# Kernel optimization log

Hardware: AMD Instinct MI355X
Metric: run time of the kernel (lower is better)

The kernel has to match this reference:

```python
import jax, jax.numpy as jnp
import numpy as np

B, F0, D = 4096, 39, 16
CROSS_LAYER_SIZE = (128, 128)


def _he_uniform(key, shape):
    fan_in = int(np.prod(shape[:-1]))
    limit = np.sqrt(6.0 / fan_in)
    return jax.random.uniform(key, shape, jnp.float32, -limit, limit)


def setup_inputs() -> dict:
    key = jax.random.key(0)
    k_x, k_f0, k_f1, k_w, k_b = jax.random.split(key, 5)
    x = jax.random.normal(k_x, (B, F0, D), dtype=jnp.float32)
    # field_nums with direct=False: [39, 128//2=64, 64]
    f0 = _he_uniform(k_f0, (F0 * F0, CROSS_LAYER_SIZE[0]))          # (1521, 128)
    f1 = _he_uniform(k_f1, (F0 * (CROSS_LAYER_SIZE[0] // 2), CROSS_LAYER_SIZE[1]))  # (2496, 128)
    out_dim = CROSS_LAYER_SIZE[0] // 2 + CROSS_LAYER_SIZE[1]        # 192
    dense_w = _he_uniform(k_w, (out_dim, 1))
    dense_b = jnp.zeros((1,), dtype=jnp.float32)
    return {"x": x, "f0": f0, "f1": f1, "dense_w": dense_w, "dense_b": dense_b}


def reference(x, f0, f1, dense_w, dense_b):
    # CIN forward (direct=False, use_bias=False, use_residual=False, relu)
    # x: (B, F0, D)
    filters = [f0, f1]
    n_layers = len(CROSS_LAYER_SIZE)
    h = x  # hidden state, (B, Fk, D)
    finals = []
    for idx, L in enumerate(CROSS_LAYER_SIZE):
        Fk = h.shape[1]
        # filter f_ has shape (F0*Fk, L) with i (field of x0) major, j (field of h) minor
        Wr = filters[idx].reshape(F0, Fk, L)
        # fused outer product + conv1d (kernel width 1 == matmul over i,j):
        # z[b, m, d] = sum_{i,j} x[b,i,d] * h[b,j,d] * W[i,j,m]
        z = jnp.einsum('bid,bjd,ijm->bmd', x, h, Wr)  # (B, L, D)
        z = jax.nn.relu(z)
        if idx != n_layers - 1:
            # split along feature-map axis: first half feeds next layer,
            # second half goes to output
            h = z[:, : L // 2, :]
            finals.append(z[:, L // 2:, :])
        else:
            finals.append(z)
    result = jnp.sum(jnp.concatenate(finals, axis=1), axis=-1)  # (B, 192)
    return result @ dense_w + dense_b  # (B, 1)
```

## Files before the change

### kernel.cpp

```cpp
#include <hip/hip_runtime.h>


typedef __attribute__((ext_vector_type(8)))  short bf16x8;
typedef __attribute__((ext_vector_type(16))) float f32x16;

static __device__ __forceinline__ unsigned short f2bf_rne(float f) {
    unsigned int u = __builtin_bit_cast(unsigned int, f);
    u = (u + 0x7FFFu + ((u >> 16) & 1u)) >> 16;
    return (unsigned short)u;
}
static __device__ __forceinline__ unsigned int pk_trunc(float a, float b) {
    unsigned int ua = __builtin_bit_cast(unsigned int, a);
    unsigned int ub = __builtin_bit_cast(unsigned int, b);
    return (ua >> 16) | (ub & 0xffff0000u);
}

__global__ __launch_bounds__(256)
void CIN_repack(const float* __restrict__ f0, const float* __restrict__ f1,
                uint4* __restrict__ ws)
{
    const int tid  = blockIdx.x * 256 + threadIdx.x;
    const int n    = tid & 127;
    const int slot = tid >> 7;
    const int half = slot & 1;
    const int kh   = (slot >> 1) & 1;
    const int ch   = slot >> 2;
    float v[8];
    if (ch < 50) {
        const int ig = ch / 5, jg = ch - ig * 5;
        const int i = ig * 4 + kh * 2 + half;
        const bool iok = (i < 39);
#pragma unroll
        for (int t = 0; t < 8; ++t) {
            const int j = jg * 8 + t;
            v[t] = (iok && j < 39) ? f0[(i * 39 + j) * 128 + n] : 0.f;
        }
    } else {
        const int c1 = ch - 50;
        const int jg = c1 / 5, ig = c1 - jg * 5;
        const int j = jg * 4 + kh * 2 + half;
#pragma unroll
        for (int t = 0; t < 8; ++t) {
            const int i = ig * 8 + t;
            v[t] = (i < 39) ? f1[(i * 64 + j) * 128 + n] : 0.f;
        }
    }
    uint4 pk;
    pk.x = (unsigned int)f2bf_rne(v[0]) | ((unsigned int)f2bf_rne(v[1]) << 16);
    pk.y = (unsigned int)f2bf_rne(v[2]) | ((unsigned int)f2bf_rne(v[3]) << 16);
    pk.z = (unsigned int)f2bf_rne(v[4]) | ((unsigned int)f2bf_rne(v[5]) << 16);
    pk.w = (unsigned int)f2bf_rne(v[6]) | ((unsigned int)f2bf_rne(v[7]) << 16);
    const int lane = half * 32 + (n & 31);
    const int cg   = n >> 5;
    ws[ch * 512 + kh * 256 + cg * 64 + lane] = pk;
}

static __device__ __forceinline__ bf16x8 build8(float xi, float4 a, float4 b) {
    union { unsigned int u[4]; bf16x8 v; } r;
    r.u[0] = pk_trunc(xi * a.x, xi * a.y);
    r.u[1] = pk_trunc(xi * a.z, xi * a.w);
    r.u[2] = pk_trunc(xi * b.x, xi * b.y);
    r.u[3] = pk_trunc(xi * b.z, xi * b.w);
    return r.v;
}

__global__ __launch_bounds__(256, 2)
void CIN_main(const float* __restrict__ x,
              const char* __restrict__ wsB,
              const float* __restrict__ dw,
              const float* __restrict__ db,
              float* __restrict__ out)
{
    __shared__ __align__(16) float xsTd[8][16][44];
    __shared__ __align__(16) float hsT[8][64][17];
    __shared__ float dws[192];
    __shared__ float red[2][2][4];

    const int tid  = threadIdx.x;
    const int w    = tid >> 6;
    const int lane = tid & 63;
    const int g    = w & 1;
    const int hh   = w >> 1;
    const int half = lane >> 5;
    const int d    = lane & 15;
    const int bsel = (lane >> 4) & 1;
    const int g4   = g * 4;

    const char* wbase = wsB + lane * 16 + hh * 2048 + 2560;
    bf16x8 Bb[2][2][2];
    auto loadBg = [&](int ch, bf16x8 (&B)[2][2]) {
        const char* p0 = wbase + (size_t)ch * 8192;
        B[0][0] = *(const bf16x8*)(p0 - 2560);
        B[0][1] = *(const bf16x8*)(p0 - 1536);
        B[1][0] = *(const bf16x8*)(p0 + 1536);
        B[1][1] = *(const bf16x8*)(p0 + 2560);
    };

    loadBg(0, Bb[0]);
    loadBg(1, Bb[1]);

    const float4* xg4 = (const float4*)(x + (size_t)blockIdx.x * 8 * 624);
    for (int e4 = tid; e4 < 1248; e4 += 256) {
        float4 v = xg4[e4];
        int bb = e4 / 156, r = e4 - bb * 156;
        int i = r >> 2, d0 = (r & 3) * 4;
        xsTd[bb][d0 + 0][i] = v.x; xsTd[bb][d0 + 1][i] = v.y;
        xsTd[bb][d0 + 2][i] = v.z; xsTd[bb][d0 + 3][i] = v.w;
    }
    if (tid < 128) { int bb = tid >> 4, dd = tid & 15; xsTd[bb][dd][39] = 0.f; }
    if (tid < 192) dws[tid] = dw[tid];
    __syncthreads();

    float4 xv[2][10];
#pragma unroll
    for (int p = 0; p < 2; ++p) {
        const float* src = &xsTd[g4 + p * 2 + bsel][d][0];
#pragma unroll
        for (int q = 0; q < 10; ++q) xv[p][q] = *(const float4*)(src + q * 4);
    }

    f32x16 acc[2][2];
#pragma unroll
    for (int p = 0; p < 2; ++p)
#pragma unroll
        for (int c = 0; c < 2; ++c)
#pragma unroll
            for (int r = 0; r < 16; ++r) acc[p][c][r] = 0.f;

    float xiv[2][2];

#pragma unroll 1
    for (int o = 0; o < 5; ++o) {
#pragma unroll
        for (int u = 0; u < 10; ++u) {
            const int ch = o * 10 + u;
            const int jg = u % 5;
            if (jg == 0) {
                const int ib = (o * 2 + u / 5) * 4;
#pragma unroll
                for (int p = 0; p < 2; ++p)
#pragma unroll
                    for (int kh = 0; kh < 2; ++kh)
                        xiv[p][kh] = xsTd[g4 + p * 2 + bsel][d][ib + kh * 2 + half];
            }
            bf16x8 A[2][2];
#pragma unroll
            for (int p = 0; p < 2; ++p)
#pragma unroll
                for (int kh = 0; kh < 2; ++kh)
                    A[p][kh] = build8(xiv[p][kh], xv[p][jg * 2], xv[p][jg * 2 + 1]);
#pragma unroll
            for (int p = 0; p < 2; ++p)
#pragma unroll
                for (int c = 0; c < 2; ++c) {
                    acc[p][c] = __builtin_amdgcn_mfma_f32_32x32x16_bf16(A[p][0], Bb[u & 1][0][c], acc[p][c], 0, 0, 0);
                    acc[p][c] = __builtin_amdgcn_mfma_f32_32x32x16_bf16(A[p][1], Bb[u & 1][1][c], acc[p][c], 0, 0, 0);
                }
            loadBg(ch + 2, Bb[u & 1]);
        }
    }

    float cs[4] = {0.f, 0.f, 0.f, 0.f};
    if (hh == 0) {
#pragma unroll
        for (int p = 0; p < 2; ++p)
#pragma unroll
            for (int c = 0; c < 2; ++c)
#pragma unroll
                for (int r = 0; r < 16; ++r) {
                    const int row = (r & 3) + 8 * (r >> 2) + 4 * half;
                    hsT[g4 + p * 2 + (row >> 4)][c * 32 + (lane & 31)][row & 15] =
                        fmaxf(acc[p][c][r], 0.f);
                }
    } else {
#pragma unroll
        for (int p = 0; p < 2; ++p)
#pragma unroll
            for (int c = 0; c < 2; ++c) {
                const float dwv = dws[c * 32 + (lane & 31)];
#pragma unroll
                for (int r = 0; r < 16; ++r) {
                    const int row = (r & 3) + 8 * (r >> 2) + 4 * half;
                    cs[p * 2 + (row >> 4)] += fmaxf(acc[p][c][r], 0.f) * dwv;
                }
            }
    }
#pragma unroll
    for (int p = 0; p < 2; ++p)
#pragma unroll
        for (int c = 0; c < 2; ++c)
#pragma unroll
            for (int r = 0; r < 16; ++r) acc[p][c][r] = 0.f;
    __syncthreads();

#pragma unroll 1
    for (int o2 = 0; o2 < 8; ++o2) {
#pragma unroll
        for (int u = 0; u < 10; ++u) {
            const int ch = 50 + o2 * 10 + u;
            const int ig2 = u % 5;
            if (ig2 == 0) {
                const int jb = (o2 * 2 + u / 5) * 4;
#pragma unroll
                for (int p = 0; p < 2; ++p)
#pragma unroll
                    for (int kh = 0; kh < 2; ++kh)
                        xiv[p][kh] = hsT[g4 + p * 2 + bsel][jb + kh * 2 + half][d];
            }
            bf16x8 A[2][2];
#pragma unroll
            for (int p = 0; p < 2; ++p)
#pragma unroll
                for (int kh = 0; kh < 2; ++kh)
                    A[p][kh] = build8(xiv[p][kh], xv[p][ig2 * 2], xv[p][ig2 * 2 + 1]);
#pragma unroll
            for (int p = 0; p < 2; ++p)
#pragma unroll
                for (int c = 0; c < 2; ++c) {
                    acc[p][c] = __builtin_amdgcn_mfma_f32_32x32x16_bf16(A[p][0], Bb[u & 1][0][c], acc[p][c], 0, 0, 0);
                    acc[p][c] = __builtin_amdgcn_mfma_f32_32x32x16_bf16(A[p][1], Bb[u & 1][1][c], acc[p][c], 0, 0, 0);
                }
            int chn = ch + 2; if (chn > 129) chn = 129;
            loadBg(chn, Bb[u & 1]);
        }
    }

#pragma unroll
    for (int p = 0; p < 2; ++p)
#pragma unroll
        for (int c = 0; c < 2; ++c) {
            const float dwv = dws[64 + (2 * hh + c) * 32 + (lane & 31)];
#pragma unroll
            for (int r = 0; r < 16; ++r) {
                const int row = (r & 3) + 8 * (r >> 2) + 4 * half;
                cs[p * 2 + (row >> 4)] += fmaxf(acc[p][c][r], 0.f) * dwv;
            }
        }
#pragma unroll
    for (int rr = 0; rr < 4; ++rr)
#pragma unroll
        for (int off = 32; off > 0; off >>= 1)
            cs[rr] += __shfl_xor(cs[rr], off, 64);
    if (lane == 0) {
#pragma unroll
        for (int rr = 0; rr < 4; ++rr) red[g][hh][rr] = cs[rr];
    }
    __syncthreads();
    if (tid < 8) {
        const int g2 = tid >> 2, rr = tid & 3;
        out[blockIdx.x * 8 + g2 * 4 + rr] = red[g2][0][rr] + red[g2][1][rr] + db[0];
    }
}

extern "C" void kernel_launch(void* const* d_in, const int* in_sizes, int n_in,
                              void* d_out, int out_size, void* d_ws, size_t ws_size,
                              hipStream_t stream)
{
    const float* x  = (const float*)d_in[0];
    const float* f0 = (const float*)d_in[1];
    const float* f1 = (const float*)d_in[2];
    const float* dw = (const float*)d_in[3];
    const float* db = (const float*)d_in[4];
    float* out = (float*)d_out;

    CIN_repack<<<dim3(260), dim3(256), 0, stream>>>(f0, f1, (uint4*)d_ws);
    CIN_main<<<dim3(512), dim3(256), 0, stream>>>(x, (const char*)d_ws, dw, db, out);
}
```

Baseline: 130.6 us.

## Switch operands from bf16 to fp16 and build A with packed half multiplies

Weights are repacked as fp16 instead of bf16, and the MFMA calls move to the f16 32x32x16 variant. x and the hidden state are staged in LDS as fp16. The A fragments are built with packed half2 multiplies instead of scalar fp32 multiplies plus truncation. This cuts VALU work per MFMA and halves LDS footprint and traffic, but products are now rounded in fp16, which risks overflow or precision loss if values are large.

```diff
diff --git a/kernel.cpp b/kernel.cpp
--- a/kernel.cpp
+++ b/kernel.cpp
@@ -1,19 +1,9 @@
 #include <hip/hip_runtime.h>
 
 
-typedef __attribute__((ext_vector_type(8)))  short bf16x8;
+typedef _Float16 h2    __attribute__((ext_vector_type(2)));
+typedef _Float16 f16x8 __attribute__((ext_vector_type(8)));
 typedef __attribute__((ext_vector_type(16))) float f32x16;
-
-static __device__ __forceinline__ unsigned short f2bf_rne(float f) {
-    unsigned int u = __builtin_bit_cast(unsigned int, f);
-    u = (u + 0x7FFFu + ((u >> 16) & 1u)) >> 16;
-    return (unsigned short)u;
-}
-static __device__ __forceinline__ unsigned int pk_trunc(float a, float b) {
-    unsigned int ua = __builtin_bit_cast(unsigned int, a);
-    unsigned int ub = __builtin_bit_cast(unsigned int, b);
-    return (ua >> 16) | (ub & 0xffff0000u);
-}
 
 __global__ __launch_bounds__(256)
 void CIN_repack(const float* __restrict__ f0, const float* __restrict__ f1,
@@ -45,23 +35,13 @@
             v[t] = (i < 39) ? f1[(i * 64 + j) * 128 + n] : 0.f;
         }
     }
-    uint4 pk;
-    pk.x = (unsigned int)f2bf_rne(v[0]) | ((unsigned int)f2bf_rne(v[1]) << 16);
-    pk.y = (unsigned int)f2bf_rne(v[2]) | ((unsigned int)f2bf_rne(v[3]) << 16);
-    pk.z = (unsigned int)f2bf_rne(v[4]) | ((unsigned int)f2bf_rne(v[5]) << 16);
-    pk.w = (unsigned int)f2bf_rne(v[6]) | ((unsigned int)f2bf_rne(v[7]) << 16);
+    union { h2 h[4]; uint4 q; } pk;
+#pragma unroll
+    for (int t = 0; t < 4; ++t)
+        pk.h[t] = h2{(_Float16)v[2 * t], (_Float16)v[2 * t + 1]};
     const int lane = half * 32 + (n & 31);
     const int cg   = n >> 5;
-    ws[ch * 512 + kh * 256 + cg * 64 + lane] = pk;
-}
-
-static __device__ __forceinline__ bf16x8 build8(float xi, float4 a, float4 b) {
-    union { unsigned int u[4]; bf16x8 v; } r;
-    r.u[0] = pk_trunc(xi * a.x, xi * a.y);
-    r.u[1] = pk_trunc(xi * a.z, xi * a.w);
-    r.u[2] = pk_trunc(xi * b.x, xi * b.y);
-    r.u[3] = pk_trunc(xi * b.z, xi * b.w);
-    return r.v;
+    ws[ch * 512 + kh * 256 + cg * 64 + lane] = pk.q;
 }
 
 __global__ __launch_bounds__(256, 2)
@@ -71,8 +51,8 @@
               const float* __restrict__ db,
               float* __restrict__ out)
 {
-    __shared__ __align__(16) float xsTd[8][16][44];
-    __shared__ __align__(16) float hsT[8][64][17];
+    __shared__ __align__(16) _Float16 xsH[8][16][64];
+    __shared__ __align__(4)  _Float16 hsH[8][64][18];
     __shared__ float dws[192];
     __shared__ float red[2][2][4];
 
@@ -87,13 +67,13 @@
     const int g4   = g * 4;
 
     const char* wbase = wsB + lane * 16 + hh * 2048 + 2560;
-    bf16x8 Bb[2][2][2];
-    auto loadBg = [&](int ch, bf16x8 (&B)[2][2]) {
+    f16x8 Bb[2][2][2];
+    auto loadBg = [&](int ch, f16x8 (&B)[2][2]) {
         const char* p0 = wbase + (size_t)ch * 8192;
-        B[0][0] = *(const bf16x8*)(p0 - 2560);
-        B[0][1] = *(const bf16x8*)(p0 - 1536);
-        B[1][0] = *(const bf16x8*)(p0 + 1536);
-        B[1][1] = *(const bf16x8*)(p0 + 2560);
+        B[0][0] = *(const f16x8*)(p0 - 2560);
+        B[0][1] = *(const f16x8*)(p0 - 1536);
+        B[1][0] = *(const f16x8*)(p0 + 1536);
+        B[1][1] = *(const f16x8*)(p0 + 2560);
     };
 
     loadBg(0, Bb[0]);
@@ -104,19 +84,24 @@
         float4 v = xg4[e4];
         int bb = e4 / 156, r = e4 - bb * 156;
         int i = r >> 2, d0 = (r & 3) * 4;
-        xsTd[bb][d0 + 0][i] = v.x; xsTd[bb][d0 + 1][i] = v.y;
-        xsTd[bb][d0 + 2][i] = v.z; xsTd[bb][d0 + 3][i] = v.w;
-    }
-    if (tid < 128) { int bb = tid >> 4, dd = tid & 15; xsTd[bb][dd][39] = 0.f; }
+        xsH[bb][d0 + 0][i] = (_Float16)v.x; xsH[bb][d0 + 1][i] = (_Float16)v.y;
+        xsH[bb][d0 + 2][i] = (_Float16)v.z; xsH[bb][d0 + 3][i] = (_Float16)v.w;
+    }
+    if (tid < 128) { int bb = tid >> 4, dd = tid & 15; xsH[bb][dd][39] = (_Float16)0.f; }
     if (tid < 192) dws[tid] = dw[tid];
     __syncthreads();
 
-    float4 xv[2][10];
+    h2 xv[2][20];
 #pragma unroll
     for (int p = 0; p < 2; ++p) {
-        const float* src = &xsTd[g4 + p * 2 + bsel][d][0];
-#pragma unroll
-        for (int q = 0; q < 10; ++q) xv[p][q] = *(const float4*)(src + q * 4);
+        const uint4* src = (const uint4*)&xsH[g4 + p * 2 + bsel][d][0];
+#pragma unroll
+        for (int q5 = 0; q5 < 5; ++q5) {
+            union { uint4 q; h2 h[4]; } u;
+            u.q = src[q5];
+#pragma unroll
+            for (int t = 0; t < 4; ++t) xv[p][q5 * 4 + t] = u.h[t];
+        }
     }
 
     f32x16 acc[2][2];
@@ -127,7 +112,7 @@
 #pragma unroll
             for (int r = 0; r < 16; ++r) acc[p][c][r] = 0.f;
 
-    float xiv[2][2];
+    h2 xiv2[2][2];
 
 #pragma unroll 1
     for (int o = 0; o < 5; ++o) {
@@ -140,21 +125,28 @@
 #pragma unroll
                 for (int p = 0; p < 2; ++p)
 #pragma unroll
-                    for (int kh = 0; kh < 2; ++kh)
-                        xiv[p][kh] = xsTd[g4 + p * 2 + bsel][d][ib + kh * 2 + half];
-            }
-            bf16x8 A[2][2];
-#pragma unroll
-            for (int p = 0; p < 2; ++p)
-#pragma unroll
-                for (int kh = 0; kh < 2; ++kh)
-                    A[p][kh] = build8(xiv[p][kh], xv[p][jg * 2], xv[p][jg * 2 + 1]);
+                    for (int kh = 0; kh < 2; ++kh) {
+                        _Float16 s = xsH[g4 + p * 2 + bsel][d][ib + kh * 2 + half];
+                        xiv2[p][kh] = h2{s, s};
+                    }
+            }
+            f16x8 A[2][2];
+#pragma unroll
+            for (int p = 0; p < 2; ++p)
+#pragma unroll
+                for (int kh = 0; kh < 2; ++kh) {
+                    union { h2 h[4]; f16x8 v; } a;
+#pragma unroll
+                    for (int q = 0; q < 4; ++q)
+                        a.h[q] = xiv2[p][kh] * xv[p][jg * 4 + q];
+                    A[p][kh] = a.v;
+                }
 #pragma unroll
             for (int p = 0; p < 2; ++p)
 #pragma unroll
                 for (int c = 0; c < 2; ++c) {
-                    acc[p][c] = __builtin_amdgcn_mfma_f32_32x32x16_bf16(A[p][0], Bb[u & 1][0][c], acc[p][c], 0, 0, 0);
-                    acc[p][c] = __builtin_amdgcn_mfma_f32_32x32x16_bf16(A[p][1], Bb[u & 1][1][c], acc[p][c], 0, 0, 0);
+                    acc[p][c] = __builtin_amdgcn_mfma_f32_32x32x16_f16(A[p][0], Bb[u & 1][0][c], acc[p][c], 0, 0, 0);
+                    acc[p][c] = __builtin_amdgcn_mfma_f32_32x32x16_f16(A[p][1], Bb[u & 1][1][c], acc[p][c], 0, 0, 0);
                 }
             loadBg(ch + 2, Bb[u & 1]);
         }
@@ -167,10 +159,11 @@
 #pragma unroll
             for (int c = 0; c < 2; ++c)
 #pragma unroll
-                for (int r = 0; r < 16; ++r) {
+                for (int r = 0; r < 16; r += 2) {
                     const int row = (r & 3) + 8 * (r >> 2) + 4 * half;
-                    hsT[g4 + p * 2 + (row >> 4)][c * 32 + (lane & 31)][row & 15] =
-                        fmaxf(acc[p][c][r], 0.f);
+                    h2 pr = h2{(_Float16)fmaxf(acc[p][c][r],     0.f),
+                               (_Float16)fmaxf(acc[p][c][r + 1], 0.f)};
+                    *(h2*)&hsH[g4 + p * 2 + (row >> 4)][c * 32 + (lane & 31)][row & 15] = pr;
                 }
     } else {
 #pragma unroll
@@ -204,21 +197,28 @@
 #pragma unroll
                 for (int p = 0; p < 2; ++p)
 #pragma unroll
-                    for (int kh = 0; kh < 2; ++kh)
-                        xiv[p][kh] = hsT[g4 + p * 2 + bsel][jb + kh * 2 + half][d];
-            }
-            bf16x8 A[2][2];
-#pragma unroll
-            for (int p = 0; p < 2; ++p)
-#pragma unroll
-                for (int kh = 0; kh < 2; ++kh)
-                    A[p][kh] = build8(xiv[p][kh], xv[p][ig2 * 2], xv[p][ig2 * 2 + 1]);
+                    for (int kh = 0; kh < 2; ++kh) {
+                        _Float16 s = hsH[g4 + p * 2 + bsel][jb + kh * 2 + half][d];
+                        xiv2[p][kh] = h2{s, s};
+                    }
+            }
+            f16x8 A[2][2];
+#pragma unroll
+            for (int p = 0; p < 2; ++p)
+#pragma unroll
+                for (int kh = 0; kh < 2; ++kh) {
+                    union { h2 h[4]; f16x8 v; } a;
+#pragma unroll
+                    for (int q = 0; q < 4; ++q)
+                        a.h[q] = xiv2[p][kh] * xv[p][ig2 * 4 + q];
+                    A[p][kh] = a.v;
+                }
 #pragma unroll
             for (int p = 0; p < 2; ++p)
 #pragma unroll
                 for (int c = 0; c < 2; ++c) {
-                    acc[p][c] = __builtin_amdgcn_mfma_f32_32x32x16_bf16(A[p][0], Bb[u & 1][0][c], acc[p][c], 0, 0, 0);
-                    acc[p][c] = __builtin_amdgcn_mfma_f32_32x32x16_bf16(A[p][1], Bb[u & 1][1][c], acc[p][c], 0, 0, 0);
+                    acc[p][c] = __builtin_amdgcn_mfma_f32_32x32x16_f16(A[p][0], Bb[u & 1][0][c], acc[p][c], 0, 0, 0);
+                    acc[p][c] = __builtin_amdgcn_mfma_f32_32x32x16_f16(A[p][1], Bb[u & 1][1][c], acc[p][c], 0, 0, 0);
                 }
             int chn = ch + 2; if (chn > 129) chn = 129;
             loadBg(chn, Bb[u & 1]);
```

New measurement: 131.3 us. No clear change (+0.5%).
